# Performance work log

Measured on AMD Instinct MI355X. Metric: run time of the kernel, lower is better.

Reference implementation:

```python
import jax, jax.numpy as jnp
import numpy as np

DIM = 128
EPS = 1e-5

def _layernorm(x, w, b, eps=EPS):
    mu = jnp.mean(x, axis=-1, keepdims=True)
    var = jnp.mean(jnp.square(x - mu), axis=-1, keepdims=True)
    return (x - mu) * jax.lax.rsqrt(var + eps) * w + b

def setup_inputs() -> dict:
    key = jax.random.key(0)
    ks = jax.random.split(key, 6)
    B, N, D = 1, 512, DIM
    x = jax.random.normal(ks[0], (B, N, N, D), dtype=jnp.float32)
    mask = jnp.ones((B, N, N), dtype=jnp.float32)
    # parameters (torch Linear weight is [out, in]; we store [in, out] for x @ W)
    lecun = 1.0 / np.sqrt(D)
    w_p_in = jax.random.normal(ks[1], (D, 2 * D), dtype=jnp.float32) * lecun
    w_g_in = jnp.zeros((D, 2 * D), dtype=jnp.float32)   # gating_init -> zeros
    w_p_out = jnp.zeros((D, D), dtype=jnp.float32)      # final_init -> zeros
    w_g_out = jnp.zeros((D, D), dtype=jnp.float32)      # gating_init -> zeros
    # use small random values instead of exact zeros to make the math non-trivial
    w_g_in = jax.random.normal(ks[2], (D, 2 * D), dtype=jnp.float32) * 0.02
    w_p_out = jax.random.normal(ks[3], (D, D), dtype=jnp.float32) * 0.02
    w_g_out = jax.random.normal(ks[4], (D, D), dtype=jnp.float32) * 0.02
    norm_in_w = jnp.ones((D,), jnp.float32)
    norm_in_b = jnp.zeros((D,), jnp.float32)
    norm_out_w = jnp.ones((D,), jnp.float32)
    norm_out_b = jnp.zeros((D,), jnp.float32)
    return {
        "x": x, "mask": mask,
        "w_p_in": w_p_in, "w_g_in": w_g_in,
        "w_p_out": w_p_out, "w_g_out": w_g_out,
        "norm_in_w": norm_in_w, "norm_in_b": norm_in_b,
        "norm_out_w": norm_out_w, "norm_out_b": norm_out_b,
    }

def reference(x, mask, w_p_in, w_g_in, w_p_out, w_g_out,
              norm_in_w, norm_in_b, norm_out_w, norm_out_b):
    # x: [B,N,N,D], mask: [B,N,N]
    xn = _layernorm(x, norm_in_w, norm_in_b)          # norm_in
    x_in = xn
    p = xn @ w_p_in                                   # [B,N,N,2D]
    g = jax.nn.sigmoid(xn @ w_g_in)
    h = p * g * mask[..., None]                       # gated + masked
    a, b = jnp.split(h.astype(jnp.float32), 2, axis=-1)  # each [B,N,N,D]
    t = jnp.einsum('bikd,bjkd->bijd', a, b)           # triangular matmul
    tn = _layernorm(t, norm_out_w, norm_out_b)        # norm_out (eps=1e-5)
    out = (tn @ w_p_out) * jax.nn.sigmoid(x_in @ w_g_out)
    return out
```

## Files before the change

### kernel.cpp

```cpp
#include <hip/hip_runtime.h>
#include <hip/hip_bf16.h>
#include <math.h>

#define NN 512
#define DD 128
#define NP (NN*NN)

#define PITCH ((size_t)(NP * 2 + 256))

typedef __attribute__((ext_vector_type(4))) float f32x4;
typedef __attribute__((ext_vector_type(8))) short bf16x8;

__device__ __forceinline__ unsigned short f2bf(float f) {
  union { float f; unsigned u; } v; v.f = f;
  unsigned r = v.u + 0x7FFFu + ((v.u >> 16) & 1u);
  return (unsigned short)(r >> 16);
}
__device__ __forceinline__ float bf2f(unsigned short h) {
  union { unsigned u; float f; } v; v.u = ((unsigned)h) << 16;
  return v.f;
}
__device__ __forceinline__ float sigmoidf_(float x) {
  return __builtin_amdgcn_rcpf(1.0f + __expf(-x));
}
__device__ __forceinline__ unsigned pkbf2(float a, float b) {
  float2 t; t.x = a; t.y = b;
  __hip_bfloat162 h = __float22bfloat162_rn(t);
  unsigned r; __builtin_memcpy(&r, &h, 4); return r;
}

__device__ __forceinline__ void gll16(void* lds, const void* g) {
  __builtin_amdgcn_global_load_lds(
      (const __attribute__((address_space(1))) void*)g,
      (__attribute__((address_space(3))) void*)lds, 16, 0, 0);
}

#define WP_P  0
#define WP_G  65536
#define WP_GO 131072
#define WP_PO 163840

__global__ __launch_bounds__(256) void kw_prep(const float* __restrict__ w_p_in,
    const float* __restrict__ w_g_in, const float* __restrict__ w_g_out,
    const float* __restrict__ w_p_out, unsigned short* __restrict__ wprep) {
  int idx = blockIdx.x * 256 + threadIdx.x;
  int n, k, base; float v;
  if (idx < 32768)       { n = idx >> 7;          k = idx & 127; v = w_p_in[k * 256 + n];  base = WP_P; }
  else if (idx < 65536)  { int e = idx - 32768;  n = e >> 7; k = e & 127; v = w_g_in[k * 256 + n];  base = WP_G; }
  else if (idx < 81920)  { int e = idx - 65536;  n = e >> 7; k = e & 127; v = w_g_out[k * 128 + n]; base = WP_GO; }
  else                   { int e = idx - 81920;  n = e >> 7; k = e & 127; v = w_p_out[k * 128 + n]; base = WP_PO; }
  int dst = base + n * 256 + ((2 * k) ^ ((n & 7) << 4));
  wprep[dst >> 1] = f2bf(v);
}

__global__ __launch_bounds__(256) void kA_ln(const float* __restrict__ x,
    const float* __restrict__ nw, const float* __restrict__ nb,
    unsigned short* __restrict__ xn_sw) {
  const int tid = threadIdx.x;
  const int l16 = tid & 15, rsub = tid >> 4;
  const int row0 = blockIdx.x * 64;
  const float4 wv0 = *(const float4*)(nw + l16 * 8);
  const float4 wv1 = *(const float4*)(nw + l16 * 8 + 4);
  const float4 bv0 = *(const float4*)(nb + l16 * 8);
  const float4 bv1 = *(const float4*)(nb + l16 * 8 + 4);
  #pragma unroll
  for (int rnd = 0; rnd < 4; ++rnd) {
    int r = row0 + rnd * 16 + rsub;
    const float* xr = x + (size_t)r * DD + l16 * 8;
    float4 v0 = *(const float4*)xr;
    float4 v1 = *(const float4*)(xr + 4);
    float s = v0.x + v0.y + v0.z + v0.w + v1.x + v1.y + v1.z + v1.w;
    float q = v0.x*v0.x + v0.y*v0.y + v0.z*v0.z + v0.w*v0.w
            + v1.x*v1.x + v1.y*v1.y + v1.z*v1.z + v1.w*v1.w;
    #pragma unroll
    for (int m = 8; m; m >>= 1) { s += __shfl_xor(s, m); q += __shfl_xor(q, m); }
    float mean = s * (1.0f / DD);
    float var = q * (1.0f / DD) - mean * mean;
    float rstd = rsqrtf(var + 1e-5f);
    uint4 pk;
    pk.x = pkbf2((v0.x - mean) * rstd * wv0.x + bv0.x, (v0.y - mean) * rstd * wv0.y + bv0.y);
    pk.y = pkbf2((v0.z - mean) * rstd * wv0.z + bv0.z, (v0.w - mean) * rstd * wv0.w + bv0.w);
    pk.z = pkbf2((v1.x - mean) * rstd * wv1.x + bv1.x, (v1.y - mean) * rstd * wv1.y + bv1.y);
    pk.w = pkbf2((v1.z - mean) * rstd * wv1.z + bv1.z, (v1.w - mean) * rstd * wv1.w + bv1.w);
    *(uint4*)((unsigned char*)xn_sw + (size_t)r * 256 + ((l16 * 16) ^ ((r & 7) << 4))) = pk;
  }
}

__global__ __launch_bounds__(256) void kB_gemm(
    const unsigned short* __restrict__ xn_sw, const float* __restrict__ mask,
    const unsigned short* __restrict__ wprep,
    unsigned char* __restrict__ a_t, unsigned char* __restrict__ b_t) {
  const int row0 = blockIdx.x * 128;
  const int tid = threadIdx.x, lane = tid & 63, wv = tid >> 6;
  const int wr = wv >> 1, wc = wv & 1;
  __shared__ __align__(16) unsigned char sxn[32768];
  __shared__ float smask[128];

  #pragma unroll
  for (int it = 0; it < 8; ++it) {
    int o = it * 4096 + tid * 16;
    gll16(sxn + o, (const unsigned char*)xn_sw + (size_t)row0 * 256 + o);
  }
  if (tid < 128) smask[tid] = mask[row0 + tid];
  __syncthreads();

  const unsigned char* wp = (const unsigned char*)wprep;

  for (int q = 0; q < 4; ++q) {
    f32x4 acc[4][4] = {};
    #pragma unroll
    for (int ks = 0; ks < 4; ++ks) {
      int kb = ks * 64 + (lane >> 4) * 16;
      bf16x8 af[4], bfr[4];
      #pragma unroll
      for (int mi = 0; mi < 4; ++mi) {
        int r = wr * 64 + mi * 16 + (lane & 15);
        af[mi] = *(const bf16x8*)(sxn + r * 256 + (kb ^ ((r & 7) << 4)));
      }
      #pragma unroll
      for (int ni = 0; ni < 2; ++ni) {
        int n = q * 64 + wc * 32 + ni * 16 + (lane & 15);
        int off = n * 256 + (kb ^ ((n & 7) << 4));
        bfr[ni]     = *(const bf16x8*)(wp + WP_P + off);
        bfr[ni + 2] = *(const bf16x8*)(wp + WP_G + off);
      }
      #pragma unroll
      for (int mi = 0; mi < 4; ++mi)
        #pragma unroll
        for (int ni = 0; ni < 4; ++ni)
          acc[mi][ni] = __builtin_amdgcn_mfma_f32_16x16x32_bf16(af[mi], bfr[ni], acc[mi][ni], 0, 0, 0);
    }
    unsigned char* dst = (q < 2) ? a_t : b_t;
    int dmin = (q & 1) * 64;
    #pragma unroll
    for (int mi = 0; mi < 4; ++mi) {
      int rq = wr * 64 + mi * 16 + (lane >> 4) * 4;
      float mk0 = smask[rq], mk1 = smask[rq + 1], mk2 = smask[rq + 2], mk3 = smask[rq + 3];
      #pragma unroll
      for (int ni = 0; ni < 2; ++ni) {
        int d = dmin + wc * 32 + ni * 16 + (lane & 15);
        uint2 pk;
        pk.x = pkbf2(acc[mi][ni][0] * sigmoidf_(acc[mi][ni + 2][0]) * mk0,
                     acc[mi][ni][1] * sigmoidf_(acc[mi][ni + 2][1]) * mk1);
        pk.y = pkbf2(acc[mi][ni][2] * sigmoidf_(acc[mi][ni + 2][2]) * mk2,
                     acc[mi][ni][3] * sigmoidf_(acc[mi][ni + 2][3]) * mk3);
        *(uint2*)(dst + (size_t)d * PITCH + (size_t)(row0 + rq) * 2) = pk;
      }
    }
  }
}

__global__ __launch_bounds__(256) void k2_einsum(
    const unsigned char* __restrict__ a_t, const unsigned char* __restrict__ b_t,
    unsigned char* __restrict__ t_out) {
  int bid = blockIdx.x;
  int wg = (bid & 7) * 256 + (bid >> 3);
  int d = wg >> 4;
  int tile = wg & 15;
  int i0 = (tile >> 2) * 128, j0 = (tile & 3) * 128;
  const int tid = threadIdx.x, lane = tid & 63, wv = tid >> 6;
  const int wr = wv >> 1, wc = wv & 1;
  __shared__ __align__(16) unsigned char sA[2][8192];
  __shared__ __align__(16) unsigned char sB[2][8192];
  const unsigned char* Abase = a_t + (size_t)d * PITCH + (size_t)i0 * 1024;
  const unsigned char* Bbase = b_t + (size_t)d * PITCH + (size_t)j0 * 1024;

  const int so0 = tid * 16;
  const int r0s = so0 >> 6, c0s = (so0 >> 4) & 3;
  const size_t ga0 = (size_t)r0s * 1024 + ((c0s ^ ((r0s >> 1) & 3)) << 4);
  const int so1 = so0 + 4096;
  const int r1s = so1 >> 6, c1s = (so1 >> 4) & 3;
  const size_t ga1 = (size_t)r1s * 1024 + ((c1s ^ ((r1s >> 1) & 3)) << 4);

  f32x4 acc[4][4] = {};
  gll16(sA[0] + so0, Abase + ga0);
  gll16(sB[0] + so0, Bbase + ga0);
  gll16(sA[0] + so1, Abase + ga1);
  gll16(sB[0] + so1, Bbase + ga1);
  __syncthreads();

  int cur = 0;
  for (int t = 0; t < 16; ++t) {
    if (t < 15) {
      int nk = (t + 1) * 64;
      gll16(sA[cur ^ 1] + so0, Abase + ga0 + nk);
      gll16(sB[cur ^ 1] + so0, Bbase + ga0 + nk);
      gll16(sA[cur ^ 1] + so1, Abase + ga1 + nk);
      gll16(sB[cur ^ 1] + so1, Bbase + ga1 + nk);
    }
    bf16x8 af[4], bfr[4];
    const int kc = lane >> 4;
    #pragma unroll
    for (int mi = 0; mi < 4; ++mi) {
      int r = wr * 64 + mi * 16 + (lane & 15);
      af[mi] = *(const bf16x8*)(sA[cur] + r * 64 + ((kc ^ ((r >> 1) & 3)) << 4));
    }
    #pragma unroll
    for (int ni = 0; ni < 4; ++ni) {
      int r = wc * 64 + ni * 16 + (lane & 15);
      bfr[ni] = *(const bf16x8*)(sB[cur] + r * 64 + ((kc ^ ((r >> 1) & 3)) << 4));
    }
    #pragma unroll
    for (int mi = 0; mi < 4; ++mi)
      #pragma unroll
      for (int ni = 0; ni < 4; ++ni)
        acc[mi][ni] = __builtin_amdgcn_mfma_f32_16x16x32_bf16(af[mi], bfr[ni], acc[mi][ni], 0, 0, 0);
    __syncthreads();
    cur ^= 1;
  }
  unsigned char* trow = t_out + (size_t)d * PITCH;
  #pragma unroll
  for (int mi = 0; mi < 4; ++mi)
    #pragma unroll
    for (int j = 0; j < 4; ++j) {
      int i = i0 + wr * 64 + mi * 16 + (lane >> 4) * 4 + j;
      #pragma unroll
      for (int ni = 0; ni < 4; ++ni) {
        int jj = j0 + wc * 64 + ni * 16 + (lane & 15);
        *(unsigned short*)(trow + ((size_t)i * 512 + jj) * 2) = f2bf(acc[mi][ni][j]);
      }
    }
}

__global__ __launch_bounds__(256) void k3_out(
    const unsigned char* __restrict__ t_in, const unsigned short* __restrict__ xn_sw,
    const unsigned short* __restrict__ wprep,
    const float* __restrict__ now, const float* __restrict__ nob,
    float* __restrict__ out) {
  const int p0 = blockIdx.x * 64;
  const int tid = threadIdx.x, lane = tid & 63, wv = tid >> 6;
  const int wr = wv >> 1, wc = wv & 1;
  __shared__ __align__(16) unsigned short sT[128 * 64];
  __shared__ __align__(16) unsigned char sTN[64 * 256];
  __shared__ __align__(16) unsigned char sxn[64 * 256];
  __shared__ float ps[4][64], pq[4][64], smean[64], srstd[64];

  #pragma unroll
  for (int it = 0; it < 4; ++it) {
    int o = it * 4096 + tid * 16;
    int dr = o >> 7, cb = o & 127;
    gll16((unsigned char*)sT + o, t_in + (size_t)dr * PITCH + (size_t)p0 * 2 + cb);
  }
  #pragma unroll
  for (int it = 0; it < 4; ++it) {
    int o = it * 4096 + tid * 16;
    gll16(sxn + o, (const unsigned char*)xn_sw + (size_t)p0 * 256 + o);
  }
  __syncthreads();
  const int p = tid & 63, dh = tid >> 6;
  {
    float s = 0.f, q = 0.f;
    #pragma unroll
    for (int dd = 0; dd < 32; ++dd) {
      float v = bf2f(sT[(dh * 32 + dd) * 64 + p]);
      s += v; q += v * v;
    }
    ps[dh][p] = s; pq[dh][p] = q;
  }
  __syncthreads();
  if (tid < 64) {
    float s = ps[0][tid] + ps[1][tid] + ps[2][tid] + ps[3][tid];
    float q = pq[0][tid] + pq[1][tid] + pq[2][tid] + pq[3][tid];
    float mean = s * (1.0f / 128.0f);
    float var = q * (1.0f / 128.0f) - mean * mean;
    smean[tid] = mean; srstd[tid] = rsqrtf(var + 1e-5f);
  }
  __syncthreads();
  {
    float mean = smean[p], rstd = srstd[p];
    #pragma unroll
    for (int e = 0; e < 16; ++e) {
      int d0 = dh * 32 + e * 2;
      float v0 = (bf2f(sT[d0 * 64 + p]) - mean) * rstd * now[d0] + nob[d0];
      float v1 = (bf2f(sT[(d0 + 1) * 64 + p]) - mean) * rstd * now[d0 + 1] + nob[d0 + 1];
      unsigned pack = pkbf2(v0, v1);
      *(unsigned*)(sTN + p * 256 + ((d0 * 2) ^ ((p & 7) << 4))) = pack;
    }
  }
  __syncthreads();
  f32x4 accP[2][4] = {}, accG[2][4] = {};
  const unsigned char* wpo = (const unsigned char*)wprep + WP_PO;
  const unsigned char* wgo = (const unsigned char*)wprep + WP_GO;
  #pragma unroll
  for (int ks = 0; ks < 4; ++ks) {
    int kb = ks * 64 + (lane >> 4) * 16;
    bf16x8 af[2], ag[2], bP[4], bG[4];
    #pragma unroll
    for (int mi = 0; mi < 2; ++mi) {
      int r = wr * 32 + mi * 16 + (lane & 15);
      int off = r * 256 + (kb ^ ((r & 7) << 4));
      af[mi] = *(const bf16x8*)(sTN + off);
      ag[mi] = *(const bf16x8*)(sxn + off);
    }
    #pragma unroll
    for (int ni = 0; ni < 4; ++ni) {
      int n = wc * 64 + ni * 16 + (lane & 15);
      int off = n * 256 + (kb ^ ((n & 7) << 4));
      bP[ni] = *(const bf16x8*)(wpo + off);
      bG[ni] = *(const bf16x8*)(wgo + off);
    }
    #pragma unroll
    for (int mi = 0; mi < 2; ++mi)
      #pragma unroll
      for (int ni = 0; ni < 4; ++ni) {
        accP[mi][ni] = __builtin_amdgcn_mfma_f32_16x16x32_bf16(af[mi], bP[ni], accP[mi][ni], 0, 0, 0);
        accG[mi][ni] = __builtin_amdgcn_mfma_f32_16x16x32_bf16(ag[mi], bG[ni], accG[mi][ni], 0, 0, 0);
      }
  }
  #pragma unroll
  for (int mi = 0; mi < 2; ++mi)
    #pragma unroll
    for (int ni = 0; ni < 4; ++ni) {
      int n = wc * 64 + ni * 16 + (lane & 15);
      int prow = wr * 32 + mi * 16 + (lane >> 4) * 4;
      #pragma unroll
      for (int j = 0; j < 4; ++j)
        out[(size_t)(p0 + prow + j) * 128 + n] = accP[mi][ni][j] * sigmoidf_(accG[mi][ni][j]);
    }
}

extern "C" void kernel_launch(void* const* d_in, const int* in_sizes, int n_in,
                              void* d_out, int out_size, void* d_ws, size_t ws_size,
                              hipStream_t stream) {
  (void)in_sizes; (void)n_in; (void)out_size; (void)ws_size;
  const float* x         = (const float*)d_in[0];
  const float* mask      = (const float*)d_in[1];
  const float* w_p_in    = (const float*)d_in[2];
  const float* w_g_in    = (const float*)d_in[3];
  const float* w_p_out   = (const float*)d_in[4];
  const float* w_g_out   = (const float*)d_in[5];
  const float* norm_in_w = (const float*)d_in[6];
  const float* norm_in_b = (const float*)d_in[7];
  const float* norm_out_w= (const float*)d_in[8];
  const float* norm_out_b= (const float*)d_in[9];
  float* out = (float*)d_out;

  unsigned char* ws = (unsigned char*)d_ws;
  const size_t SLAB = (size_t)128 * PITCH;
  unsigned char* a_t    = ws;
  unsigned char* b_t    = ws + SLAB;
  unsigned char* t_buf  = ws + 2 * SLAB;
  unsigned short* xn_sw = (unsigned short*)(ws + 3 * SLAB);
  unsigned short* wprep = (unsigned short*)(ws + 3 * SLAB + (size_t)NP * 256);

  kw_prep<<<384, 256, 0, stream>>>(w_p_in, w_g_in, w_g_out, w_p_out, wprep);
  kA_ln<<<4096, 256, 0, stream>>>(x, norm_in_w, norm_in_b, xn_sw);
  kB_gemm<<<2048, 256, 0, stream>>>(xn_sw, mask, wprep, a_t, b_t);
  k2_einsum<<<2048, 256, 0, stream>>>(a_t, b_t, t_buf);
  k3_out<<<4096, 256, 0, stream>>>(t_buf, xn_sw, wprep, norm_out_w, norm_out_b, out);
}
```

Measured before the change: 284.3 us.

## Stage GEMM and einsum epilogues through LDS for coalesced 16-byte stores

The projection GEMM now splits its four output quarters across a second grid dimension, so each block computes one quarter. Its gated and masked results are transposed through a swizzled shared-memory tile and then written with 16-byte coalesced stores. The einsum kernel likewise stages its bf16 output tile in shared memory, replacing scattered 2-byte global stores with 16-byte row stores. This targets poorly coalesced epilogue writes. In exchange, each GEMM block reloads the same input rows from global memory four times, and both kernels use more shared memory and add barriers.

```diff
diff --git a/kernel.cpp b/kernel.cpp
--- a/kernel.cpp
+++ b/kernel.cpp
@@ -90,10 +90,12 @@
     const unsigned short* __restrict__ xn_sw, const float* __restrict__ mask,
     const unsigned short* __restrict__ wprep,
     unsigned char* __restrict__ a_t, unsigned char* __restrict__ b_t) {
-  const int row0 = blockIdx.x * 128;
+  const int q = blockIdx.x;
+  const int row0 = blockIdx.y * 128;
   const int tid = threadIdx.x, lane = tid & 63, wv = tid >> 6;
   const int wr = wv >> 1, wc = wv & 1;
   __shared__ __align__(16) unsigned char sxn[32768];
+  __shared__ __align__(16) unsigned char sepi[16384];
   __shared__ float smask[128];
 
   #pragma unroll
@@ -106,47 +108,54 @@
 
   const unsigned char* wp = (const unsigned char*)wprep;
 
-  for (int q = 0; q < 4; ++q) {
-    f32x4 acc[4][4] = {};
-    #pragma unroll
-    for (int ks = 0; ks < 4; ++ks) {
-      int kb = ks * 64 + (lane >> 4) * 16;
-      bf16x8 af[4], bfr[4];
-      #pragma unroll
-      for (int mi = 0; mi < 4; ++mi) {
-        int r = wr * 64 + mi * 16 + (lane & 15);
-        af[mi] = *(const bf16x8*)(sxn + r * 256 + (kb ^ ((r & 7) << 4)));
-      }
-      #pragma unroll
-      for (int ni = 0; ni < 2; ++ni) {
-        int n = q * 64 + wc * 32 + ni * 16 + (lane & 15);
-        int off = n * 256 + (kb ^ ((n & 7) << 4));
-        bfr[ni]     = *(const bf16x8*)(wp + WP_P + off);
-        bfr[ni + 2] = *(const bf16x8*)(wp + WP_G + off);
-      }
-      #pragma unroll
-      for (int mi = 0; mi < 4; ++mi)
-        #pragma unroll
-        for (int ni = 0; ni < 4; ++ni)
-          acc[mi][ni] = __builtin_amdgcn_mfma_f32_16x16x32_bf16(af[mi], bfr[ni], acc[mi][ni], 0, 0, 0);
-    }
-    unsigned char* dst = (q < 2) ? a_t : b_t;
-    int dmin = (q & 1) * 64;
+  f32x4 acc[4][4] = {};
+  #pragma unroll
+  for (int ks = 0; ks < 4; ++ks) {
+    int kb = ks * 64 + (lane >> 4) * 16;
+    bf16x8 af[4], bfr[4];
     #pragma unroll
     for (int mi = 0; mi < 4; ++mi) {
-      int rq = wr * 64 + mi * 16 + (lane >> 4) * 4;
-      float mk0 = smask[rq], mk1 = smask[rq + 1], mk2 = smask[rq + 2], mk3 = smask[rq + 3];
-      #pragma unroll
-      for (int ni = 0; ni < 2; ++ni) {
-        int d = dmin + wc * 32 + ni * 16 + (lane & 15);
-        uint2 pk;
-        pk.x = pkbf2(acc[mi][ni][0] * sigmoidf_(acc[mi][ni + 2][0]) * mk0,
-                     acc[mi][ni][1] * sigmoidf_(acc[mi][ni + 2][1]) * mk1);
-        pk.y = pkbf2(acc[mi][ni][2] * sigmoidf_(acc[mi][ni + 2][2]) * mk2,
-                     acc[mi][ni][3] * sigmoidf_(acc[mi][ni + 2][3]) * mk3);
-        *(uint2*)(dst + (size_t)d * PITCH + (size_t)(row0 + rq) * 2) = pk;
-      }
-    }
+      int r = wr * 64 + mi * 16 + (lane & 15);
+      af[mi] = *(const bf16x8*)(sxn + r * 256 + (kb ^ ((r & 7) << 4)));
+    }
+    #pragma unroll
+    for (int ni = 0; ni < 2; ++ni) {
+      int n = q * 64 + wc * 32 + ni * 16 + (lane & 15);
+      int off = n * 256 + (kb ^ ((n & 7) << 4));
+      bfr[ni]     = *(const bf16x8*)(wp + WP_P + off);
+      bfr[ni + 2] = *(const bf16x8*)(wp + WP_G + off);
+    }
+    #pragma unroll
+    for (int mi = 0; mi < 4; ++mi)
+      #pragma unroll
+      for (int ni = 0; ni < 4; ++ni)
+        acc[mi][ni] = __builtin_amdgcn_mfma_f32_16x16x32_bf16(af[mi], bfr[ni], acc[mi][ni], 0, 0, 0);
+  }
+
+  #pragma unroll
+  for (int mi = 0; mi < 4; ++mi) {
+    int rq = wr * 64 + mi * 16 + (lane >> 4) * 4;
+    float mk0 = smask[rq], mk1 = smask[rq + 1], mk2 = smask[rq + 2], mk3 = smask[rq + 3];
+    #pragma unroll
+    for (int ni = 0; ni < 2; ++ni) {
+      int drel = wc * 32 + ni * 16 + (lane & 15);
+      uint2 pk;
+      pk.x = pkbf2(acc[mi][ni][0] * sigmoidf_(acc[mi][ni + 2][0]) * mk0,
+                   acc[mi][ni][1] * sigmoidf_(acc[mi][ni + 2][1]) * mk1);
+      pk.y = pkbf2(acc[mi][ni][2] * sigmoidf_(acc[mi][ni + 2][2]) * mk2,
+                   acc[mi][ni][3] * sigmoidf_(acc[mi][ni + 2][3]) * mk3);
+      *(uint2*)(sepi + drel * 256 + ((rq * 2) ^ ((drel & 7) << 4))) = pk;
+    }
+  }
+  __syncthreads();
+  unsigned char* dst = (q < 2) ? a_t : b_t;
+  const int dmin = (q & 1) * 64;
+  #pragma unroll
+  for (int it = 0; it < 4; ++it) {
+    int idx = it * 256 + tid;
+    int dr = idx >> 4, ch = idx & 15;
+    uint4 v = *(const uint4*)(sepi + dr * 256 + ((ch * 16) ^ ((dr & 7) << 4)));
+    *(uint4*)(dst + (size_t)(dmin + dr) * PITCH + (size_t)(row0 + ch * 8) * 2) = v;
   }
 }
 
@@ -160,8 +169,9 @@
   int i0 = (tile >> 2) * 128, j0 = (tile & 3) * 128;
   const int tid = threadIdx.x, lane = tid & 63, wv = tid >> 6;
   const int wr = wv >> 1, wc = wv & 1;
-  __shared__ __align__(16) unsigned char sA[2][8192];
-  __shared__ __align__(16) unsigned char sB[2][8192];
+  __shared__ __align__(16) unsigned char smem[32768];
+  unsigned char* sA0 = smem;
+  unsigned char* sB0 = smem + 16384;
   const unsigned char* Abase = a_t + (size_t)d * PITCH + (size_t)i0 * 1024;
   const unsigned char* Bbase = b_t + (size_t)d * PITCH + (size_t)j0 * 1024;
 
@@ -173,32 +183,34 @@
   const size_t ga1 = (size_t)r1s * 1024 + ((c1s ^ ((r1s >> 1) & 3)) << 4);
 
   f32x4 acc[4][4] = {};
-  gll16(sA[0] + so0, Abase + ga0);
-  gll16(sB[0] + so0, Bbase + ga0);
-  gll16(sA[0] + so1, Abase + ga1);
-  gll16(sB[0] + so1, Bbase + ga1);
+  gll16(sA0 + so0, Abase + ga0);
+  gll16(sB0 + so0, Bbase + ga0);
+  gll16(sA0 + so1, Abase + ga1);
+  gll16(sB0 + so1, Bbase + ga1);
   __syncthreads();
 
   int cur = 0;
   for (int t = 0; t < 16; ++t) {
     if (t < 15) {
       int nk = (t + 1) * 64;
-      gll16(sA[cur ^ 1] + so0, Abase + ga0 + nk);
-      gll16(sB[cur ^ 1] + so0, Bbase + ga0 + nk);
-      gll16(sA[cur ^ 1] + so1, Abase + ga1 + nk);
-      gll16(sB[cur ^ 1] + so1, Bbase + ga1 + nk);
+      int nb_ = (cur ^ 1) * 8192;
+      gll16(sA0 + nb_ + so0, Abase + ga0 + nk);
+      gll16(sB0 + nb_ + so0, Bbase + ga0 + nk);
+      gll16(sA0 + nb_ + so1, Abase + ga1 + nk);
+      gll16(sB0 + nb_ + so1, Bbase + ga1 + nk);
     }
     bf16x8 af[4], bfr[4];
     const int kc = lane >> 4;
+    int cb = cur * 8192;
     #pragma unroll
     for (int mi = 0; mi < 4; ++mi) {
       int r = wr * 64 + mi * 16 + (lane & 15);
-      af[mi] = *(const bf16x8*)(sA[cur] + r * 64 + ((kc ^ ((r >> 1) & 3)) << 4));
+      af[mi] = *(const bf16x8*)(sA0 + cb + r * 64 + ((kc ^ ((r >> 1) & 3)) << 4));
     }
     #pragma unroll
     for (int ni = 0; ni < 4; ++ni) {
       int r = wc * 64 + ni * 16 + (lane & 15);
-      bfr[ni] = *(const bf16x8*)(sB[cur] + r * 64 + ((kc ^ ((r >> 1) & 3)) << 4));
+      bfr[ni] = *(const bf16x8*)(sB0 + cb + r * 64 + ((kc ^ ((r >> 1) & 3)) << 4));
     }
     #pragma unroll
     for (int mi = 0; mi < 4; ++mi)
@@ -208,18 +220,27 @@
     __syncthreads();
     cur ^= 1;
   }
+
+  #pragma unroll
+  for (int mi = 0; mi < 4; ++mi)
+    #pragma unroll
+    for (int j = 0; j < 4; ++j) {
+      int il = wr * 64 + mi * 16 + (lane >> 4) * 4 + j;
+      #pragma unroll
+      for (int ni = 0; ni < 4; ++ni) {
+        int jl = wc * 64 + ni * 16 + (lane & 15);
+        *(unsigned short*)(smem + il * 256 + ((jl * 2) ^ ((il & 7) << 4))) = f2bf(acc[mi][ni][j]);
+      }
+    }
+  __syncthreads();
   unsigned char* trow = t_out + (size_t)d * PITCH;
   #pragma unroll
-  for (int mi = 0; mi < 4; ++mi)
-    #pragma unroll
-    for (int j = 0; j < 4; ++j) {
-      int i = i0 + wr * 64 + mi * 16 + (lane >> 4) * 4 + j;
-      #pragma unroll
-      for (int ni = 0; ni < 4; ++ni) {
-        int jj = j0 + wc * 64 + ni * 16 + (lane & 15);
-        *(unsigned short*)(trow + ((size_t)i * 512 + jj) * 2) = f2bf(acc[mi][ni][j]);
-      }
-    }
+  for (int rr = 0; rr < 8; ++rr) {
+    int idx = rr * 256 + tid;
+    int il = idx >> 4, ch = idx & 15;
+    uint4 v = *(const uint4*)(smem + il * 256 + ((ch * 16) ^ ((il & 7) << 4)));
+    *(uint4*)(trow + (size_t)(i0 + il) * 1024 + (size_t)(j0 + ch * 8) * 2) = v;
+  }
 }
 
 __global__ __launch_bounds__(256) void k3_out(
@@ -345,7 +366,8 @@
 
   kw_prep<<<384, 256, 0, stream>>>(w_p_in, w_g_in, w_g_out, w_p_out, wprep);
   kA_ln<<<4096, 256, 0, stream>>>(x, norm_in_w, norm_in_b, xn_sw);
-  kB_gemm<<<2048, 256, 0, stream>>>(xn_sw, mask, wprep, a_t, b_t);
+  dim3 gb(4, 2048);
+  kB_gemm<<<gb, 256, 0, stream>>>(xn_sw, mask, wprep, a_t, b_t);
   k2_einsum<<<2048, 256, 0, stream>>>(a_t, b_t, t_buf);
   k3_out<<<4096, 256, 0, stream>>>(t_buf, xn_sw, wprep, norm_out_w, norm_out_b, out);
 }
```

Measured after the change: 252.0 us. 1.13x faster.
